# Kernel tuning notes

Measured on AMD Instinct MI355X. Metric: run time of the kernel, lower is better.

## Reference

```python
import jax, jax.numpy as jnp
import numpy as np

# dims: B batch, CIN/COUT channels, K kernel, H/W spatial, S stride, P padding
B, CIN, COUT, K, H, W, S, P = 8, 16, 64, 3, 32, 32, 1, 1
ALPHA, R, N_EKV, VT, VD = 0.05625, 0.1, 1.5, 0.025, 0.1


def setup_inputs() -> dict:
    key = jax.random.key(0)
    k1, k2 = jax.random.split(key)
    x = jax.random.normal(k1, (B, CIN, H, W), dtype=jnp.float32)
    # torch init: uniform_(theta, 1.0, 8.0)
    theta = jax.random.uniform(k2, (COUT, CIN * K * K), dtype=jnp.float32, minval=1.0, maxval=8.0)
    scale = jnp.array(1.0, dtype=jnp.float32)
    return {"x": x, "theta": theta, "scale": scale}


def _unfold(x, k, s, p):
    # torch.nn.Unfold: patches flattened channel-major as (C, kh, kw)
    b, c, h, w = x.shape
    ho = (h + 2 * p - k) // s + 1
    wo = (w + 2 * p - k) // s + 1
    xp = jnp.pad(x, ((0, 0), (0, 0), (p, p), (p, p)))
    patches = jnp.stack(
        [xp[:, :, i:i + ho * s:s, j:j + wo * s:s] for i in range(k) for j in range(k)],
        axis=2,
    )  # (B, C, K*K, Ho, Wo)
    return patches.reshape(b, c * k * k, ho * wo), ho, wo


def _log1p_exp_stable_sq(a):
    # clamp to [-50, 20] then softplus; squared (EKV f)
    a = jnp.clip(a, -50.0, 20.0)
    sp = jnp.log1p(jnp.exp(a))
    return sp * sp


def reference(x, theta, scale):
    theta = jnp.clip(theta, 1.0, 8.0)  # mirrors theta.data.clamp_(1, 8)
    vg, ho, wo = _unfold(x, K, S, P)          # (B, Cin*K^2, L)
    vg = vg[:, None, :, :]                    # (B, 1, Cin*K^2, L)
    vth = theta[None, :, :, None]             # (1, Cout, Cin*K^2, 1)
    denom = 2.0 * N_EKV * VT
    term1 = _log1p_exp_stable_sq((vg - vth) / denom)
    term2 = _log1p_exp_stable_sq((vg - vth - VD) / denom)
    currents = jnp.clip(ALPHA * (term1 - term2), 0.0, None)
    i_k = jnp.sum(currents, axis=2)           # reduce over Cin*K^2 -> (B, Cout, L)
    v_out = i_k * R * scale
    return v_out.reshape(x.shape[0], COUT, ho, wo)
```

## Files before the change

### kernel.cpp

```cpp
#include <hip/hip_runtime.h>

#define BB 8
#define CIN 16
#define COUT 64
#define HH 32
#define WW 32

#define SCALE_C 19.235933878519388f
#define K2E 0.26359713811472845f
#define B_HI 28.85390081777927f
#define WINLO_S (-13.849872392533959f)
#define OUT_CONST (0.4804530139182014f * 0.05625f * 0.1f)

#define EXP2F(x) __builtin_amdgcn_exp2f(x)
#define LOG2F(x) __builtin_amdgcn_logf(x)

#define XROWS 10
#define XCOLS 34
#define XPLANE (XROWS * XCOLS)
#define PHASE_CINS 8
#define STAGE_ELEMS (PHASE_CINS * XPLANE)

__device__ __forceinline__ void compute9(const float* v, const float4* th03,
                                         const float4* th47, float th8, float* acc) {
    float th[9] = {th03->x, th03->y, th03->z, th03->w,
                   th47->x, th47->y, th47->z, th47->w, th8};
#pragma unroll
    for (int k = 0; k < 9; ++k) {
        float b1 = v[k] - th[k];
        if (__any(b1 > WINLO_S)) {
            float e1 = EXP2F(b1);
            float e2 = e1 * K2E;
            float l1 = fminf(LOG2F(1.0f + e1), B_HI);
            float l2 = fminf(LOG2F(1.0f + e2), B_HI);
            float a = acc[k % 3];
            a = fmaf(l1, l1, a);
            a = fmaf(-l2, l2, a);
            acc[k % 3] = a;
        }
    }
}

__global__ __launch_bounds__(256, 8) void ekv_kernel(const float* __restrict__ x,
                                                     const float* __restrict__ theta,
                                                     const float* __restrict__ scale,
                                                     float* __restrict__ out) {
    int bid = blockIdx.x;
    int b = bid & 7;
    int tile = (bid >> 3) & 3;
    int co = (bid >> 8) * 8 + ((bid >> 5) & 7);

    int t = threadIdx.x;
    int ow = t & 31;
    int ohl = t >> 5;
    int oh = tile * 8 + ohl;

    __shared__ __align__(16) float s_x[STAGE_ELEMS];
    __shared__ __align__(16) float s_th[CIN * 12];

    if (t < CIN * 12) {
        int cin = t / 12;
        int j = t - cin * 12;
        float v = 0.0f;
        if (j < 9) v = fminf(fmaxf(theta[co * (CIN * 9) + cin * 9 + j], 1.0f), 8.0f) * SCALE_C;
        s_th[t] = v;
    }

    const float* xb = x + (size_t)b * (CIN * HH * WW);
    float acc[3] = {0.0f, 0.0f, 0.0f};
    float sc = scale[0] * (OUT_CONST);

    int pixbase = ohl * XCOLS + ow;

#pragma unroll 1
    for (int phase = 0; phase < 2; ++phase) {
        int cinBase = phase * PHASE_CINS;
        if (phase) __syncthreads();

#pragma unroll 1
        for (int i = t; i < STAGE_ELEMS; i += 256) {
            int cinL = i / XPLANE;
            int rem = i - cinL * XPLANE;
            int r = rem / XCOLS;
            int c = rem - r * XCOLS;
            int gy = tile * 8 + r - 1;
            int gx = c - 1;
            float v = 0.0f;
            if ((unsigned)gy < HH && (unsigned)gx < WW)
                v = xb[((cinBase + cinL) * HH + gy) * WW + gx] * SCALE_C;
            s_x[i] = v;
        }
        __syncthreads();

        float va[9], vb[9];
        {
            const float* p = s_x + pixbase;
#pragma unroll
            for (int dy = 0; dy < 3; ++dy)
#pragma unroll
                for (int dx = 0; dx < 3; ++dx) va[dy * 3 + dx] = p[dy * XCOLS + dx];
        }
#pragma unroll 1
        for (int cl = 0; cl < PHASE_CINS; cl += 2) {
            {
                const float* p = s_x + (cl + 1) * XPLANE + pixbase;
#pragma unroll
                for (int dy = 0; dy < 3; ++dy)
#pragma unroll
                    for (int dx = 0; dx < 3; ++dx) vb[dy * 3 + dx] = p[dy * XCOLS + dx];
            }
            {
                int cin = cinBase + cl;
                const float4* th03 = (const float4*)&s_th[cin * 12];
                const float4* th47 = th03 + 1;
                compute9(va, th03, th47, s_th[cin * 12 + 8], acc);
            }
            {
                int nc = cl + 2 < PHASE_CINS ? cl + 2 : PHASE_CINS - 1;
                const float* p = s_x + nc * XPLANE + pixbase;
#pragma unroll
                for (int dy = 0; dy < 3; ++dy)
#pragma unroll
                    for (int dx = 0; dx < 3; ++dx) va[dy * 3 + dx] = p[dy * XCOLS + dx];
            }
            {
                int cin = cinBase + cl + 1;
                const float4* th03 = (const float4*)&s_th[cin * 12];
                const float4* th47 = th03 + 1;
                compute9(vb, th03, th47, s_th[cin * 12 + 8], acc);
            }
        }
    }

    out[(((size_t)b * COUT + co) * HH + oh) * WW + ow] =
        (acc[0] + acc[1] + acc[2]) * sc;
}

extern "C" void kernel_launch(void* const* d_in, const int* in_sizes, int n_in,
                              void* d_out, int out_size, void* d_ws, size_t ws_size,
                              hipStream_t stream) {
    const float* x = (const float*)d_in[0];
    const float* theta = (const float*)d_in[1];
    const float* scale = (const float*)d_in[2];
    float* out = (float*)d_out;
    (void)d_ws; (void)ws_size; (void)in_sizes; (void)n_in; (void)out_size;

    ekv_kernel<<<BB * 4 * COUT, 256, 0, stream>>>(x, theta, scale, out);
}
```

Measured before the change: 78.63 us.

## Presort thresholds per channel and break early using block max of input

A new pre-kernel clamps and scales theta, then sorts each output channel's taps by threshold within each 8-channel phase. Each tap is stored with its precomputed shared-memory offset. The main kernel reduces the maximum staged input per block and walks the sorted taps. It stops once a threshold exceeds max+window, which replaces the per-tap wave-vote skip with one uniform early exit. This saves dead exp/log work and divergence checks, at the cost of an extra launch, a workspace buffer and indirect LDS loads.

New measurement: 88.89 us. 1.13x slower.

```diff
diff --git a/kernel.cpp b/kernel.cpp
--- a/kernel.cpp
+++ b/kernel.cpp
@@ -21,28 +21,52 @@
 #define PHASE_CINS 8
 #define STAGE_ELEMS (PHASE_CINS * XPLANE)
 
-__device__ __forceinline__ void compute9(const float* v, const float4* th03,
-                                         const float4* th47, float th8, float* acc) {
-    float th[9] = {th03->x, th03->y, th03->z, th03->w,
-                   th47->x, th47->y, th47->z, th47->w, th8};
-#pragma unroll
-    for (int k = 0; k < 9; ++k) {
-        float b1 = v[k] - th[k];
-        if (__any(b1 > WINLO_S)) {
-            float e1 = EXP2F(b1);
-            float e2 = e1 * K2E;
-            float l1 = fminf(LOG2F(1.0f + e1), B_HI);
-            float l2 = fminf(LOG2F(1.0f + e2), B_HI);
-            float a = acc[k % 3];
-            a = fmaf(l1, l1, a);
-            a = fmaf(-l2, l2, a);
-            acc[k % 3] = a;
+struct Tap {
+    float th;
+    int off4;
+};
+
+__global__ __launch_bounds__(192) void sort_kernel(const float* __restrict__ theta,
+                                                   Tap* __restrict__ taps) {
+    int co = blockIdx.x;
+    int j = threadIdx.x;
+    __shared__ float s_thv[144];
+    float thv = 0.0f;
+    int off4 = 0;
+    if (j < 144) {
+        int cin = j / 9, k = j - cin * 9;
+        int dy = k / 3, dx = k - dy * 3;
+        thv = fminf(fmaxf(theta[co * 144 + j], 1.0f), 8.0f) * SCALE_C;
+        off4 = ((cin & 7) * XPLANE + dy * XCOLS + dx) * 4;
+        s_thv[j] = thv;
+    }
+    __syncthreads();
+    if (j < 144) {
+        int base = (j / 72) * 72;
+        int rank = 0;
+        for (int i = 0; i < 72; ++i) {
+            float o = s_thv[base + i];
+            rank += (o < thv) || (o == thv && (base + i) < j);
         }
+        Tap e;
+        e.th = thv;
+        e.off4 = off4;
+        taps[co * 144 + base + rank] = e;
     }
 }
 
+__device__ __forceinline__ void eval_tap(float v, float th, float& acc) {
+    float b1 = v - th;
+    float e1 = EXP2F(b1);
+    float e2 = e1 * K2E;
+    float l1 = fminf(LOG2F(1.0f + e1), B_HI);
+    float l2 = fminf(LOG2F(1.0f + e2), B_HI);
+    acc = fmaf(l1, l1, acc);
+    acc = fmaf(-l2, l2, acc);
+}
+
 __global__ __launch_bounds__(256, 8) void ekv_kernel(const float* __restrict__ x,
-                                                     const float* __restrict__ theta,
+                                                     const Tap* __restrict__ taps,
                                                      const float* __restrict__ scale,
                                                      float* __restrict__ out) {
     int bid = blockIdx.x;
@@ -56,27 +80,20 @@
     int oh = tile * 8 + ohl;
 
     __shared__ __align__(16) float s_x[STAGE_ELEMS];
-    __shared__ __align__(16) float s_th[CIN * 12];
-
-    if (t < CIN * 12) {
-        int cin = t / 12;
-        int j = t - cin * 12;
-        float v = 0.0f;
-        if (j < 9) v = fminf(fmaxf(theta[co * (CIN * 9) + cin * 9 + j], 1.0f), 8.0f) * SCALE_C;
-        s_th[t] = v;
-    }
+    __shared__ float s_red[4];
 
     const float* xb = x + (size_t)b * (CIN * HH * WW);
-    float acc[3] = {0.0f, 0.0f, 0.0f};
-    float sc = scale[0] * (OUT_CONST);
+    const Tap* tp = taps + co * 144;
+    const char* s_xb = (const char*)s_x;
+    int pix4 = (ohl * XCOLS + ow) * 4;
 
-    int pixbase = ohl * XCOLS + ow;
+    float acc0 = 0.0f, acc1 = 0.0f;
 
 #pragma unroll 1
     for (int phase = 0; phase < 2; ++phase) {
-        int cinBase = phase * PHASE_CINS;
         if (phase) __syncthreads();
 
+        float m = -1e30f;
 #pragma unroll 1
         for (int i = t; i < STAGE_ELEMS; i += 256) {
             int cinL = i / XPLANE;
@@ -87,53 +104,33 @@
             int gx = c - 1;
             float v = 0.0f;
             if ((unsigned)gy < HH && (unsigned)gx < WW)
-                v = xb[((cinBase + cinL) * HH + gy) * WW + gx] * SCALE_C;
+                v = xb[((phase * PHASE_CINS + cinL) * HH + gy) * WW + gx] * SCALE_C;
             s_x[i] = v;
+            m = fmaxf(m, v);
         }
+#pragma unroll
+        for (int d2 = 32; d2; d2 >>= 1) m = fmaxf(m, __shfl_xor(m, d2));
+        if ((t & 63) == 0) s_red[t >> 6] = m;
         __syncthreads();
+        m = fmaxf(fmaxf(s_red[0], s_red[1]), fmaxf(s_red[2], s_red[3]));
+        float cut = __builtin_amdgcn_readfirstlane(m) - WINLO_S;
 
-        float va[9], vb[9];
-        {
-            const float* p = s_x + pixbase;
-#pragma unroll
-            for (int dy = 0; dy < 3; ++dy)
-#pragma unroll
-                for (int dx = 0; dx < 3; ++dx) va[dy * 3 + dx] = p[dy * XCOLS + dx];
-        }
+        const Tap* tpp = tp + phase * 72;
 #pragma unroll 1
-        for (int cl = 0; cl < PHASE_CINS; cl += 2) {
-            {
-                const float* p = s_x + (cl + 1) * XPLANE + pixbase;
-#pragma unroll
-                for (int dy = 0; dy < 3; ++dy)
-#pragma unroll
-                    for (int dx = 0; dx < 3; ++dx) vb[dy * 3 + dx] = p[dy * XCOLS + dx];
-            }
-            {
-                int cin = cinBase + cl;
-                const float4* th03 = (const float4*)&s_th[cin * 12];
-                const float4* th47 = th03 + 1;
-                compute9(va, th03, th47, s_th[cin * 12 + 8], acc);
-            }
-            {
-                int nc = cl + 2 < PHASE_CINS ? cl + 2 : PHASE_CINS - 1;
-                const float* p = s_x + nc * XPLANE + pixbase;
-#pragma unroll
-                for (int dy = 0; dy < 3; ++dy)
-#pragma unroll
-                    for (int dx = 0; dx < 3; ++dx) va[dy * 3 + dx] = p[dy * XCOLS + dx];
-            }
-            {
-                int cin = cinBase + cl + 1;
-                const float4* th03 = (const float4*)&s_th[cin * 12];
-                const float4* th47 = th03 + 1;
-                compute9(vb, th03, th47, s_th[cin * 12 + 8], acc);
-            }
+        for (int i = 0; i < 72; i += 2) {
+            Tap e0 = tpp[i];
+            if (e0.th >= cut) break;
+            float v0 = *(const float*)(s_xb + (pix4 + e0.off4));
+            eval_tap(v0, e0.th, acc0);
+            Tap e1 = tpp[i + 1];
+            if (e1.th >= cut) break;
+            float v1 = *(const float*)(s_xb + (pix4 + e1.off4));
+            eval_tap(v1, e1.th, acc1);
         }
     }
 
-    out[(((size_t)b * COUT + co) * HH + oh) * WW + ow] =
-        (acc[0] + acc[1] + acc[2]) * sc;
+    float sc = scale[0] * (OUT_CONST);
+    out[(((size_t)b * COUT + co) * HH + oh) * WW + ow] = (acc0 + acc1) * sc;
 }
 
 extern "C" void kernel_launch(void* const* d_in, const int* in_sizes, int n_in,
@@ -143,7 +140,10 @@
     const float* theta = (const float*)d_in[1];
     const float* scale = (const float*)d_in[2];
     float* out = (float*)d_out;
-    (void)d_ws; (void)ws_size; (void)in_sizes; (void)n_in; (void)out_size;
 
-    ekv_kernel<<<BB * 4 * COUT, 256, 0, stream>>>(x, theta, scale, out);
+    Tap* taps = (Tap*)d_ws;
+    (void)ws_size; (void)in_sizes; (void)n_in; (void)out_size;
+
+    sort_kernel<<<COUT, 192, 0, stream>>>(theta, taps);
+    ekv_kernel<<<BB * 4 * COUT, 256, 0, stream>>>(x, taps, scale, out);
 }
```
